# Kernel optimization log

Hardware: AMD Instinct MI355X
Metric: run time of the kernel (lower is better)

Reference implementation:

```python
import jax, jax.numpy as jnp
import numpy as np

H, D = 16, 64  # num_attention_heads, attention_head_size
BASE = 10000.0

def _rope(q, k, seq_len):
    # RotaryPositionalEmbedding: inv_freq over arange(0, D, 2); emb = cat(freqs, freqs)
    inv_freq = 1.0 / (BASE ** (jnp.arange(0, D, 2, dtype=jnp.float32) / D))  # [D/2]=32
    pos = jnp.arange(seq_len, dtype=jnp.float32)
    freqs = jnp.outer(pos, inv_freq)            # [S, 32]; equals cos_emb[..., :d]
    cos, sin = jnp.cos(freqs), jnp.sin(freqs)   # [S, 32]
    d = D // 2                                   # 32: only first half of head dim rotated
    half = d // 2                                # 16: internal rotate-half within rot part
    def rot(x):  # x: [B, H, S, D]
        xr, xp = x[..., :d], x[..., d:]
        swapped = jnp.concatenate([xr[..., half:], xr[..., :half]], axis=-1)
        xr2 = xr * cos - swapped * sin
        return jnp.concatenate([xr2, xp], axis=-1)
    return rot(q), rot(k)

def setup_inputs() -> dict:
    key = jax.random.key(0)
    ks = jax.random.split(key, 9)
    B, S, E = 2, 2048, 1024
    std = 0.02  # initializer_range
    inp = {"hidden_states": jax.random.normal(ks[0], (B, S, E), jnp.float32)}
    for i, n in enumerate(["q", "k", "v", "d"]):
        inp[f"W{n}"] = jax.random.normal(ks[1 + 2 * i], (E, E), jnp.float32) * std
        inp[f"b{n}"] = jnp.zeros((E,), jnp.float32)
    return inp

def reference(hidden_states, Wq, bq, Wk, bk, Wv, bv, Wd, bd):
    B, S, E = hidden_states.shape
    def heads(x):  # [B,S,E] -> [B,H,S,D]
        return x.reshape(B, S, H, D).transpose(0, 2, 1, 3)
    q = heads(hidden_states @ Wq + bq)
    k = heads(hidden_states @ Wk + bk)
    v = heads(hidden_states @ Wv + bv)
    q, k = _rope(q, k, S)
    scores = jnp.einsum("bhqd,bhkd->bhqk", q, k) / jnp.sqrt(jnp.float32(D))
    causal = jnp.tril(jnp.ones((S, S), dtype=bool))
    scores = jnp.where(causal, scores, -jnp.inf)
    probs = jax.nn.softmax(scores, axis=-1)
    ctx = jnp.einsum("bhqk,bhkd->bhqd", probs, v)
    ctx = ctx.transpose(0, 2, 1, 3).reshape(B, S, E)
    return ctx @ Wd + bd
```

## Files before the change

kernel.cpp:

```cpp
#include <hip/hip_runtime.h>
#include <stdint.h>

typedef __bf16 bf8 __attribute__((ext_vector_type(8)));
typedef float f4 __attribute__((ext_vector_type(4)));
typedef float f16v __attribute__((ext_vector_type(16)));
typedef unsigned short us8 __attribute__((ext_vector_type(8)));
typedef unsigned short us4 __attribute__((ext_vector_type(4)));

#define MFMA16(a, b, c) __builtin_amdgcn_mfma_f32_16x16x32_bf16(a, b, c, 0, 0, 0)
#define MFMA32(a, b, c) __builtin_amdgcn_mfma_f32_32x32x16_bf16(a, b, c, 0, 0, 0)

__device__ __forceinline__ unsigned short f2b(float f) {
  union { float f; unsigned u; } x; x.f = f;
  unsigned u = x.u;
  u += 0x7fffu + ((u >> 16) & 1u);
  return (unsigned short)(u >> 16);
}

__device__ __forceinline__ unsigned pk2(float a, float b) {
  union { float f; unsigned u; } ua, ub; ua.f = a; ub.f = b;
  return __builtin_amdgcn_perm(ub.u + 0x8000u, ua.u + 0x8000u, 0x07060302u);
}

__global__ __launch_bounds__(256) void cvt_bf16_kernel(
    const float* __restrict__ x, unsigned short* __restrict__ y) {
  int i = blockIdx.x * 256 + threadIdx.x;
  float4 v = ((const float4*)x)[i];
  us4 r = { f2b(v.x), f2b(v.y), f2b(v.z), f2b(v.w) };
  *(us4*)(y + (size_t)i * 4) = r;
}

__global__ __launch_bounds__(256) void transpose_cvt4_kernel(
    const float* __restrict__ W0, const float* __restrict__ W1,
    const float* __restrict__ W2, const float* __restrict__ W3,
    unsigned short* __restrict__ T0, unsigned short* __restrict__ T1,
    unsigned short* __restrict__ T2, unsigned short* __restrict__ T3) {
  const float* W; unsigned short* Wt;
  if (blockIdx.z == 0)      { W = W0; Wt = T0; }
  else if (blockIdx.z == 1) { W = W1; Wt = T1; }
  else if (blockIdx.z == 2) { W = W2; Wt = T2; }
  else                      { W = W3; Wt = T3; }
  __shared__ float tile[32][33];
  int tx = threadIdx.x & 31, ty = threadIdx.x >> 5;
  int kb = blockIdx.x * 32, nb = blockIdx.y * 32;
#pragma unroll
  for (int j = 0; j < 32; j += 8)
    tile[ty + j][tx] = W[(size_t)(kb + ty + j) * 1024 + nb + tx];
  __syncthreads();
#pragma unroll
  for (int j = 0; j < 32; j += 8)
    Wt[(size_t)(nb + ty + j) * 1024 + kb + tx] = f2b(tile[tx][ty + j]);
}

#define LDSK 40

__global__ __launch_bounds__(256) void gemm_qkv_kernel(
    const unsigned short* __restrict__ X,
    const unsigned short* __restrict__ Wqt, const unsigned short* __restrict__ Wkt,
    const unsigned short* __restrict__ Wvt,
    const float* __restrict__ bq, const float* __restrict__ bk,
    const float* __restrict__ bv,
    unsigned short* __restrict__ Qo, unsigned short* __restrict__ Ko,
    unsigned short* __restrict__ Vo) {
  const unsigned short* Wt; const float* bias; unsigned short* out;
  if (blockIdx.z == 0)      { Wt = Wqt; bias = bq; out = Qo; }
  else if (blockIdx.z == 1) { Wt = Wkt; bias = bk; out = Ko; }
  else                      { Wt = Wvt; bias = bv; out = Vo; }

  __shared__ unsigned short As[128 * LDSK];
  __shared__ unsigned short Bs[128 * LDSK];
  const int t = threadIdx.x;
  const int wave = t >> 6, lane = t & 63, quad = lane >> 4, l16 = lane & 15;
  const int wm = (wave >> 1) * 64, wn = (wave & 1) * 64;
  const int m0 = blockIdx.y * 128, n0 = blockIdx.x * 128;

  f4 acc[4][4];
#pragma unroll
  for (int mi = 0; mi < 4; ++mi)
#pragma unroll
    for (int ni = 0; ni < 4; ++ni) acc[mi][ni] = (f4)0.0f;

  for (int k0 = 0; k0 < 1024; k0 += 32) {
    __syncthreads();
#pragma unroll
    for (int it = 0; it < 2; ++it) {
      int chunk = t + it * 256;
      int row = chunk >> 2, c8 = (chunk & 3) * 8;
      *(us8*)&As[row * LDSK + c8] =
          *(const us8*)&X[(size_t)(m0 + row) * 1024 + k0 + c8];
      *(us8*)&Bs[row * LDSK + c8] =
          *(const us8*)&Wt[(size_t)(n0 + row) * 1024 + k0 + c8];
    }
    __syncthreads();
    bf8 a[4], b[4];
#pragma unroll
    for (int mi = 0; mi < 4; ++mi)
      a[mi] = *(const bf8*)&As[(wm + mi * 16 + l16) * LDSK + quad * 8];
#pragma unroll
    for (int ni = 0; ni < 4; ++ni)
      b[ni] = *(const bf8*)&Bs[(wn + ni * 16 + l16) * LDSK + quad * 8];
#pragma unroll
    for (int mi = 0; mi < 4; ++mi)
#pragma unroll
      for (int ni = 0; ni < 4; ++ni)
        acc[mi][ni] = MFMA16(a[mi], b[ni], acc[mi][ni]);
  }

  float biasv[4];
#pragma unroll
  for (int ni = 0; ni < 4; ++ni) biasv[ni] = bias[n0 + wn + ni * 16 + l16];

  if (blockIdx.z < 2) {
    const float kr = 13.287712379549449f / 32.0f;
    const float f0 = exp2f(-(float)l16 * kr);
    const float f1 = exp2f(-(float)(l16 + 16) * kr);
    const float qs = (blockIdx.z == 0) ? 0.18033688011112042f : 1.0f;
#pragma unroll
    for (int mi = 0; mi < 4; ++mi) {
#pragma unroll
      for (int r = 0; r < 4; ++r) {
        int m = m0 + wm + mi * 16 + quad * 4 + r;
        float s = (float)(m & 2047);
        float s0, c0, s1, c1;
        __sincosf(s * f0, &s0, &c0);
        __sincosf(s * f1, &s1, &c1);
        float v0 = acc[mi][0][r] + biasv[0];
        float v1 = acc[mi][1][r] + biasv[1];
        acc[mi][0][r] = (v0 * c0 - v1 * s0) * qs;
        acc[mi][1][r] = (v1 * c1 - v0 * s1) * qs;
        acc[mi][2][r] = (acc[mi][2][r] + biasv[2]) * qs;
        acc[mi][3][r] = (acc[mi][3][r] + biasv[3]) * qs;
      }
    }
#pragma unroll
    for (int ni = 0; ni < 4; ++ni) {
      int n = n0 + wn + ni * 16 + l16;
      int h = n >> 6, d = n & 63;
#pragma unroll
      for (int mi = 0; mi < 4; ++mi) {
#pragma unroll
        for (int r = 0; r < 4; ++r) {
          int m = m0 + wm + mi * 16 + quad * 4 + r;
          int b_ = m >> 11, s = m & 2047;
          out[(size_t)(((b_ << 4) | h) * 2048 + s) * 64 + d] = f2b(acc[mi][ni][r]);
        }
      }
    }
  } else {
#pragma unroll
    for (int ni = 0; ni < 4; ++ni) {
      int n = n0 + wn + ni * 16 + l16;
      int h = n >> 6, d = n & 63;
#pragma unroll
      for (int mi = 0; mi < 4; ++mi) {
        int m = m0 + wm + mi * 16 + quad * 4;
        int b_ = m >> 11, s = m & 2047;
        us4 w = { f2b(acc[mi][ni][0] + biasv[ni]), f2b(acc[mi][ni][1] + biasv[ni]),
                  f2b(acc[mi][ni][2] + biasv[ni]), f2b(acc[mi][ni][3] + biasv[ni]) };
        *(us4*)&out[((size_t)(((b_ << 4) | h) * 64 + d)) * 2048 + s] = w;
      }
    }
  }
}

#define PST 72

__global__ __launch_bounds__(256, 2) void flash_attn_kernel(
    const unsigned short* __restrict__ Q, const unsigned short* __restrict__ K,
    const unsigned short* __restrict__ Vt, unsigned short* __restrict__ ctx) {
  __shared__ unsigned short PsT[4][32 * PST];

  const int t = threadIdx.x;
  const int wave = t >> 6, lane = t & 63;
  const int l32 = lane & 31, hl = lane >> 5;

  const int id = blockIdx.x;
  const int bh = id & 31;
  const int j = id >> 5;
  const int qt = (j >> 3) ? (15 - (j & 7)) : (j & 7);
  const int qbase = qt * 128;
  const int b = bh >> 4, h = bh & 15;

  const unsigned short* Qh = Q + (size_t)bh * 2048 * 64;
  const unsigned short* Kh = K + (size_t)bh * 2048 * 64;
  const unsigned short* Vh = Vt + (size_t)bh * 64 * 2048;

  const int wrow0 = qbase + wave * 32;
  const int q = wrow0 + l32;

  bf8 qb[4];
#pragma unroll
  for (int c = 0; c < 4; ++c)
    qb[c] = *(const bf8*)&Qh[(size_t)q * 64 + c * 16 + hl * 8];

  f16v o0 = (f16v)0.0f, o1 = (f16v)0.0f;
  float mrow = -3e38f, lrow = 0.0f;

  unsigned short* myP = &PsT[wave][0];
  const int nkw = (wrow0 >> 6) + 1;

  bf8 kfA[2][4], vfA[2][4], kfB[2][4], vfB[2][4];

  auto loadK = [&](bf8 (&kf)[2][4], int k0) {
#pragma unroll
    for (int mt = 0; mt < 2; ++mt)
#pragma unroll
      for (int c = 0; c < 4; ++c)
        kf[mt][c] = *(const bf8*)&Kh[(size_t)(k0 + mt * 32 + l32) * 64 + c * 16 + hl * 8];
  };
  auto loadV = [&](bf8 (&vf)[2][4], int k0) {
#pragma unroll
    for (int dt = 0; dt < 2; ++dt)
#pragma unroll
      for (int c = 0; c < 4; ++c)
        vf[dt][c] = *(const bf8*)&Vh[(size_t)(dt * 32 + l32) * 2048 + k0 + c * 16 + hl * 8];
  };

  auto step = [&](int k0, bf8 (&kf)[2][4], bf8 (&vf)[2][4]) {
    f16v s0 = (f16v)0.0f, s1 = (f16v)0.0f;
#pragma unroll
    for (int c = 0; c < 4; ++c) {
      s0 = MFMA32(kf[0][c], qb[c], s0);
      s1 = MFMA32(kf[1][c], qb[c], s1);
    }
    if (k0 + 64 > wrow0) {
#pragma unroll
      for (int g = 0; g < 4; ++g)
#pragma unroll
        for (int i = 0; i < 4; ++i) {
          int kk = k0 + g * 8 + hl * 4 + i;
          if (kk > q) s0[g * 4 + i] = -3e38f;
          if (kk + 32 > q) s1[g * 4 + i] = -3e38f;
        }
    }
    float mx = fmaxf(s0[0], s1[0]);
#pragma unroll
    for (int i = 1; i < 16; ++i) mx = fmaxf(mx, fmaxf(s0[i], s1[i]));
    mx = fmaxf(mx, __shfl_xor(mx, 32));
    float mn = fmaxf(mrow, mx);
    float al = exp2f(mrow - mn);
    mrow = mn;
    float sum = 0.0f;
#pragma unroll
    for (int g = 0; g < 4; ++g) {
      float p0 = exp2f(s0[g * 4 + 0] - mn), p1 = exp2f(s0[g * 4 + 1] - mn);
      float p2 = exp2f(s0[g * 4 + 2] - mn), p3 = exp2f(s0[g * 4 + 3] - mn);
      sum += (p0 + p1) + (p2 + p3);
      uint2 w = { pk2(p0, p1), pk2(p2, p3) };
      *(uint2*)&myP[l32 * PST + g * 8 + hl * 4] = w;
      float r0 = exp2f(s1[g * 4 + 0] - mn), r1 = exp2f(s1[g * 4 + 1] - mn);
      float r2 = exp2f(s1[g * 4 + 2] - mn), r3 = exp2f(s1[g * 4 + 3] - mn);
      sum += (r0 + r1) + (r2 + r3);
      uint2 w2 = { pk2(r0, r1), pk2(r2, r3) };
      *(uint2*)&myP[l32 * PST + 32 + g * 8 + hl * 4] = w2;
    }
#pragma unroll
    for (int i = 0; i < 16; ++i) { o0[i] *= al; o1[i] *= al; }
    asm volatile("s_waitcnt lgkmcnt(0)" ::: "memory");
    bf8 pb[4];
#pragma unroll
    for (int c = 0; c < 4; ++c)
      pb[c] = *(const bf8*)&myP[l32 * PST + c * 16 + hl * 8];
#pragma unroll
    for (int c = 0; c < 4; ++c) {
      o0 = MFMA32(vf[0][c], pb[c], o0);
      o1 = MFMA32(vf[1][c], pb[c], o1);
    }
    sum += __shfl_xor(sum, 32);
    lrow = lrow * al + sum;
  };

  loadK(kfA, 0); loadV(vfA, 0);
  int kt = 0;
  while (true) {
    if (kt + 1 < nkw) { loadK(kfB, (kt + 1) * 64); loadV(vfB, (kt + 1) * 64); }
    step(kt * 64, kfA, vfA);
    ++kt; if (kt >= nkw) break;
    if (kt + 1 < nkw) { loadK(kfA, (kt + 1) * 64); loadV(vfA, (kt + 1) * 64); }
    step(kt * 64, kfB, vfB);
    ++kt; if (kt >= nkw) break;
  }

  float inv = 1.0f / lrow;
#pragma unroll
  for (int g = 0; g < 4; ++g) {
    int d0 = g * 8 + hl * 4;
    us4 w0 = { f2b(o0[g * 4 + 0] * inv), f2b(o0[g * 4 + 1] * inv),
               f2b(o0[g * 4 + 2] * inv), f2b(o0[g * 4 + 3] * inv) };
    *(us4*)&ctx[((size_t)(b * 2048 + q)) * 1024 + h * 64 + d0] = w0;
    us4 w1 = { f2b(o1[g * 4 + 0] * inv), f2b(o1[g * 4 + 1] * inv),
               f2b(o1[g * 4 + 2] * inv), f2b(o1[g * 4 + 3] * inv) };
    *(us4*)&ctx[((size_t)(b * 2048 + q)) * 1024 + h * 64 + 32 + d0] = w1;
  }
}

__global__ __launch_bounds__(256) void gemm_out_kernel(
    const unsigned short* __restrict__ A,
    const unsigned short* __restrict__ Wt,
    const float* __restrict__ bias, float* __restrict__ out) {
  __shared__ unsigned short As[128 * LDSK];
  __shared__ unsigned short Bs[128 * LDSK];
  const int t = threadIdx.x;
  const int wave = t >> 6, lane = t & 63, quad = lane >> 4, l16 = lane & 15;
  const int wm = (wave >> 1) * 64, wn = (wave & 1) * 64;
  const int m0 = blockIdx.y * 128, n0 = blockIdx.x * 128;

  f4 acc[4][4];
#pragma unroll
  for (int mi = 0; mi < 4; ++mi)
#pragma unroll
    for (int ni = 0; ni < 4; ++ni) acc[mi][ni] = (f4)0.0f;

  for (int k0 = 0; k0 < 1024; k0 += 32) {
    __syncthreads();
#pragma unroll
    for (int it = 0; it < 2; ++it) {
      int chunk = t + it * 256;
      int row = chunk >> 2, c8 = (chunk & 3) * 8;
      *(us8*)&As[row * LDSK + c8] =
          *(const us8*)&A[(size_t)(m0 + row) * 1024 + k0 + c8];
      *(us8*)&Bs[row * LDSK + c8] =
          *(const us8*)&Wt[(size_t)(n0 + row) * 1024 + k0 + c8];
    }
    __syncthreads();
    bf8 a[4], b[4];
#pragma unroll
    for (int mi = 0; mi < 4; ++mi)
      a[mi] = *(const bf8*)&As[(wm + mi * 16 + l16) * LDSK + quad * 8];
#pragma unroll
    for (int ni = 0; ni < 4; ++ni)
      b[ni] = *(const bf8*)&Bs[(wn + ni * 16 + l16) * LDSK + quad * 8];
#pragma unroll
    for (int mi = 0; mi < 4; ++mi)
#pragma unroll
      for (int ni = 0; ni < 4; ++ni)
        acc[mi][ni] = MFMA16(a[mi], b[ni], acc[mi][ni]);
  }
#pragma unroll
  for (int ni = 0; ni < 4; ++ni) {
    int n = n0 + wn + ni * 16 + l16;
    float bv_ = bias[n];
#pragma unroll
    for (int mi = 0; mi < 4; ++mi) {
#pragma unroll
      for (int r = 0; r < 4; ++r) {
        int m = m0 + wm + mi * 16 + quad * 4 + r;
        out[(size_t)m * 1024 + n] = acc[mi][ni][r] + bv_;
      }
    }
  }
}

extern "C" void kernel_launch(void* const* d_in, const int* in_sizes, int n_in,
                              void* d_out, int out_size, void* d_ws, size_t ws_size,
                              hipStream_t stream) {
  const float* hidden = (const float*)d_in[0];
  const float* Wq = (const float*)d_in[1];
  const float* bq = (const float*)d_in[2];
  const float* Wk = (const float*)d_in[3];
  const float* bk = (const float*)d_in[4];
  const float* Wv = (const float*)d_in[5];
  const float* bv = (const float*)d_in[6];
  const float* Wd = (const float*)d_in[7];
  const float* bd = (const float*)d_in[8];
  float* out = (float*)d_out;

  char* ws = (char*)d_ws;
  unsigned short* Xb  = (unsigned short*)(ws);
  unsigned short* Wqt = (unsigned short*)(ws + ( 8ull << 20));
  unsigned short* Wkt = (unsigned short*)(ws + (10ull << 20));
  unsigned short* Wvt = (unsigned short*)(ws + (12ull << 20));
  unsigned short* Wdt = (unsigned short*)(ws + (14ull << 20));
  unsigned short* Qb  = (unsigned short*)(ws + (16ull << 20));
  unsigned short* Kb  = (unsigned short*)(ws + (24ull << 20));
  unsigned short* Vb  = (unsigned short*)(ws + (32ull << 20));
  unsigned short* Cb  = (unsigned short*)(ws + (40ull << 20));

  cvt_bf16_kernel<<<4096, 256, 0, stream>>>(hidden, Xb);
  transpose_cvt4_kernel<<<dim3(32, 32, 4), 256, 0, stream>>>(
      Wq, Wk, Wv, Wd, Wqt, Wkt, Wvt, Wdt);
  gemm_qkv_kernel<<<dim3(8, 32, 3), 256, 0, stream>>>(
      Xb, Wqt, Wkt, Wvt, bq, bk, bv, Qb, Kb, Vb);
  flash_attn_kernel<<<512, 256, 0, stream>>>(Qb, Kb, Vb, Cb);
  gemm_out_kernel<<<dim3(8, 32), 256, 0, stream>>>(Cb, Wdt, bd, out);
}
```

Measured before the change: 236.1 us.

## Use direct global-to-LDS loads in GEMMs, shuffle P in registers, smaller out tiles

Both GEMM kernels now stage tiles through global_load_lds (direct global-to-LDS DMA) instead of going through registers, and drop LDS padding. The flash attention kernel removes its LDS round trip for the probability matrix by rebuilding the MFMA B operand with cross-half-wave shuffles. It also loads V just in time rather than double-buffering it, which reduces register pressure. The output GEMM switches to 64x128 tiles to launch twice as many blocks. The unpadded LDS layout risks bank conflicts, and V loads are no longer hidden behind a full step.

```diff
diff --git a/kernel.cpp b/kernel.cpp
--- a/kernel.cpp
+++ b/kernel.cpp
@@ -20,6 +20,12 @@
 __device__ __forceinline__ unsigned pk2(float a, float b) {
   union { float f; unsigned u; } ua, ub; ua.f = a; ub.f = b;
   return __builtin_amdgcn_perm(ub.u + 0x8000u, ua.u + 0x8000u, 0x07060302u);
+}
+
+__device__ __forceinline__ void gload16(const void* g, void* l) {
+  __builtin_amdgcn_global_load_lds(
+      (const __attribute__((address_space(1))) void*)g,
+      (__attribute__((address_space(3))) void*)l, 16, 0, 0);
 }
 
 __global__ __launch_bounds__(256) void cvt_bf16_kernel(
@@ -52,8 +58,6 @@
     Wt[(size_t)(nb + ty + j) * 1024 + kb + tx] = f2b(tile[tx][ty + j]);
 }
 
-#define LDSK 40
-
 __global__ __launch_bounds__(256) void gemm_qkv_kernel(
     const unsigned short* __restrict__ X,
     const unsigned short* __restrict__ Wqt, const unsigned short* __restrict__ Wkt,
@@ -67,8 +71,8 @@
   else if (blockIdx.z == 1) { Wt = Wkt; bias = bk; out = Ko; }
   else                      { Wt = Wvt; bias = bv; out = Vo; }
 
-  __shared__ unsigned short As[128 * LDSK];
-  __shared__ unsigned short Bs[128 * LDSK];
+  __shared__ unsigned short As[128 * 32];
+  __shared__ unsigned short Bs[128 * 32];
   const int t = threadIdx.x;
   const int wave = t >> 6, lane = t & 63, quad = lane >> 4, l16 = lane & 15;
   const int wm = (wave >> 1) * 64, wn = (wave & 1) * 64;
@@ -84,21 +88,21 @@
     __syncthreads();
 #pragma unroll
     for (int it = 0; it < 2; ++it) {
-      int chunk = t + it * 256;
-      int row = chunk >> 2, c8 = (chunk & 3) * 8;
-      *(us8*)&As[row * LDSK + c8] =
-          *(const us8*)&X[(size_t)(m0 + row) * 1024 + k0 + c8];
-      *(us8*)&Bs[row * LDSK + c8] =
-          *(const us8*)&Wt[(size_t)(n0 + row) * 1024 + k0 + c8];
+      int chunk = it * 256 + wave * 64 + lane;
+      int row = chunk >> 2, c = chunk & 3;
+      gload16(&X[(size_t)(m0 + row) * 1024 + k0 + c * 8],
+              &As[(size_t)(it * 256 + wave * 64) * 8]);
+      gload16(&Wt[(size_t)(n0 + row) * 1024 + k0 + c * 8],
+              &Bs[(size_t)(it * 256 + wave * 64) * 8]);
     }
     __syncthreads();
     bf8 a[4], b[4];
 #pragma unroll
     for (int mi = 0; mi < 4; ++mi)
-      a[mi] = *(const bf8*)&As[(wm + mi * 16 + l16) * LDSK + quad * 8];
+      a[mi] = *(const bf8*)&As[(wm + mi * 16 + l16) * 32 + quad * 8];
 #pragma unroll
     for (int ni = 0; ni < 4; ++ni)
-      b[ni] = *(const bf8*)&Bs[(wn + ni * 16 + l16) * LDSK + quad * 8];
+      b[ni] = *(const bf8*)&Bs[(wn + ni * 16 + l16) * 32 + quad * 8];
 #pragma unroll
     for (int mi = 0; mi < 4; ++mi)
 #pragma unroll
@@ -163,16 +167,12 @@
   }
 }
 
-#define PST 72
-
 __global__ __launch_bounds__(256, 2) void flash_attn_kernel(
     const unsigned short* __restrict__ Q, const unsigned short* __restrict__ K,
     const unsigned short* __restrict__ Vt, unsigned short* __restrict__ ctx) {
-  __shared__ unsigned short PsT[4][32 * PST];
-
   const int t = threadIdx.x;
-  const int wave = t >> 6, lane = t & 63;
-  const int l32 = lane & 31, hl = lane >> 5;
+  const int lane = t & 63;
+  const int wave = t >> 6, l32 = lane & 31, hl = lane >> 5;
 
   const int id = blockIdx.x;
   const int bh = id & 31;
@@ -195,11 +195,9 @@
 
   f16v o0 = (f16v)0.0f, o1 = (f16v)0.0f;
   float mrow = -3e38f, lrow = 0.0f;
-
-  unsigned short* myP = &PsT[wave][0];
   const int nkw = (wrow0 >> 6) + 1;
 
-  bf8 kfA[2][4], vfA[2][4], kfB[2][4], vfB[2][4];
+  bf8 kfA[2][4], kfB[2][4], vf[2][4];
 
   auto loadK = [&](bf8 (&kf)[2][4], int k0) {
 #pragma unroll
@@ -208,7 +206,7 @@
       for (int c = 0; c < 4; ++c)
         kf[mt][c] = *(const bf8*)&Kh[(size_t)(k0 + mt * 32 + l32) * 64 + c * 16 + hl * 8];
   };
-  auto loadV = [&](bf8 (&vf)[2][4], int k0) {
+  auto loadV = [&](int k0) {
 #pragma unroll
     for (int dt = 0; dt < 2; ++dt)
 #pragma unroll
@@ -216,7 +214,7 @@
         vf[dt][c] = *(const bf8*)&Vh[(size_t)(dt * 32 + l32) * 2048 + k0 + c * 16 + hl * 8];
   };
 
-  auto step = [&](int k0, bf8 (&kf)[2][4], bf8 (&vf)[2][4]) {
+  auto step = [&](int k0, bf8 (&kf)[2][4]) {
     f16v s0 = (f16v)0.0f, s1 = (f16v)0.0f;
 #pragma unroll
     for (int c = 0; c < 4; ++c) {
@@ -240,44 +238,48 @@
     float mn = fmaxf(mrow, mx);
     float al = exp2f(mrow - mn);
     mrow = mn;
+    uint2 pd2[8];
     float sum = 0.0f;
 #pragma unroll
     for (int g = 0; g < 4; ++g) {
       float p0 = exp2f(s0[g * 4 + 0] - mn), p1 = exp2f(s0[g * 4 + 1] - mn);
       float p2 = exp2f(s0[g * 4 + 2] - mn), p3 = exp2f(s0[g * 4 + 3] - mn);
       sum += (p0 + p1) + (p2 + p3);
-      uint2 w = { pk2(p0, p1), pk2(p2, p3) };
-      *(uint2*)&myP[l32 * PST + g * 8 + hl * 4] = w;
+      pd2[g].x = pk2(p0, p1); pd2[g].y = pk2(p2, p3);
       float r0 = exp2f(s1[g * 4 + 0] - mn), r1 = exp2f(s1[g * 4 + 1] - mn);
       float r2 = exp2f(s1[g * 4 + 2] - mn), r3 = exp2f(s1[g * 4 + 3] - mn);
       sum += (r0 + r1) + (r2 + r3);
-      uint2 w2 = { pk2(r0, r1), pk2(r2, r3) };
-      *(uint2*)&myP[l32 * PST + 32 + g * 8 + hl * 4] = w2;
+      pd2[4 + g].x = pk2(r0, r1); pd2[4 + g].y = pk2(r2, r3);
     }
 #pragma unroll
     for (int i = 0; i < 16; ++i) { o0[i] *= al; o1[i] *= al; }
-    asm volatile("s_waitcnt lgkmcnt(0)" ::: "memory");
-    bf8 pb[4];
-#pragma unroll
-    for (int c = 0; c < 4; ++c)
-      pb[c] = *(const bf8*)&myP[l32 * PST + c * 16 + hl * 8];
 #pragma unroll
     for (int c = 0; c < 4; ++c) {
-      o0 = MFMA32(vf[0][c], pb[c], o0);
-      o1 = MFMA32(vf[1][c], pb[c], o1);
+      uint2 lo = pd2[2 * c], hi = pd2[2 * c + 1];
+      unsigned sx = hl ? lo.x : hi.x, sy = hl ? lo.y : hi.y;
+      unsigned rx = __shfl_xor(sx, 32), ry = __shfl_xor(sy, 32);
+      union { uint4 u; bf8 v; } fr;
+      fr.u.x = hl ? rx : lo.x;
+      fr.u.y = hl ? ry : lo.y;
+      fr.u.z = hl ? hi.x : rx;
+      fr.u.w = hl ? hi.y : ry;
+      o0 = MFMA32(vf[0][c], fr.v, o0);
+      o1 = MFMA32(vf[1][c], fr.v, o1);
     }
     sum += __shfl_xor(sum, 32);
     lrow = lrow * al + sum;
   };
 
-  loadK(kfA, 0); loadV(vfA, 0);
+  loadK(kfA, 0);
   int kt = 0;
   while (true) {
-    if (kt + 1 < nkw) { loadK(kfB, (kt + 1) * 64); loadV(vfB, (kt + 1) * 64); }
-    step(kt * 64, kfA, vfA);
+    loadV(kt * 64);
+    if (kt + 1 < nkw) loadK(kfB, (kt + 1) * 64);
+    step(kt * 64, kfA);
     ++kt; if (kt >= nkw) break;
-    if (kt + 1 < nkw) { loadK(kfA, (kt + 1) * 64); loadV(vfA, (kt + 1) * 64); }
-    step(kt * 64, kfB, vfB);
+    loadV(kt * 64);
+    if (kt + 1 < nkw) loadK(kfA, (kt + 1) * 64);
+    step(kt * 64, kfB);
     ++kt; if (kt >= nkw) break;
   }
 
@@ -298,40 +300,44 @@
     const unsigned short* __restrict__ A,
     const unsigned short* __restrict__ Wt,
     const float* __restrict__ bias, float* __restrict__ out) {
-  __shared__ unsigned short As[128 * LDSK];
-  __shared__ unsigned short Bs[128 * LDSK];
+  __shared__ unsigned short As[64 * 32];
+  __shared__ unsigned short Bs[128 * 32];
   const int t = threadIdx.x;
   const int wave = t >> 6, lane = t & 63, quad = lane >> 4, l16 = lane & 15;
-  const int wm = (wave >> 1) * 64, wn = (wave & 1) * 64;
-  const int m0 = blockIdx.y * 128, n0 = blockIdx.x * 128;
-
-  f4 acc[4][4];
-#pragma unroll
-  for (int mi = 0; mi < 4; ++mi)
+  const int wm = (wave & 1) * 32, wn = (wave >> 1) * 64;
+  const int m0 = blockIdx.y * 64, n0 = blockIdx.x * 128;
+
+  f4 acc[2][4];
+#pragma unroll
+  for (int mi = 0; mi < 2; ++mi)
 #pragma unroll
     for (int ni = 0; ni < 4; ++ni) acc[mi][ni] = (f4)0.0f;
 
   for (int k0 = 0; k0 < 1024; k0 += 32) {
     __syncthreads();
-#pragma unroll
-    for (int it = 0; it < 2; ++it) {
-      int chunk = t + it * 256;
-      int row = chunk >> 2, c8 = (chunk & 3) * 8;
-      *(us8*)&As[row * LDSK + c8] =
-          *(const us8*)&A[(size_t)(m0 + row) * 1024 + k0 + c8];
-      *(us8*)&Bs[row * LDSK + c8] =
-          *(const us8*)&Wt[(size_t)(n0 + row) * 1024 + k0 + c8];
+    {
+      int chunk = wave * 64 + lane;
+      int row = chunk >> 2, c = chunk & 3;
+      gload16(&A[(size_t)(m0 + row) * 1024 + k0 + c * 8],
+              &As[(size_t)(wave * 64) * 8]);
+#pragma unroll
+      for (int it = 0; it < 2; ++it) {
+        int ch = it * 256 + wave * 64 + lane;
+        int rw = ch >> 2, cc = ch & 3;
+        gload16(&Wt[(size_t)(n0 + rw) * 1024 + k0 + cc * 8],
+                &Bs[(size_t)(it * 256 + wave * 64) * 8]);
+      }
     }
     __syncthreads();
-    bf8 a[4], b[4];
-#pragma unroll
-    for (int mi = 0; mi < 4; ++mi)
-      a[mi] = *(const bf8*)&As[(wm + mi * 16 + l16) * LDSK + quad * 8];
+    bf8 a[2], b[4];
+#pragma unroll
+    for (int mi = 0; mi < 2; ++mi)
+      a[mi] = *(const bf8*)&As[(wm + mi * 16 + l16) * 32 + quad * 8];
 #pragma unroll
     for (int ni = 0; ni < 4; ++ni)
-      b[ni] = *(const bf8*)&Bs[(wn + ni * 16 + l16) * LDSK + quad * 8];
-#pragma unroll
-    for (int mi = 0; mi < 4; ++mi)
+      b[ni] = *(const bf8*)&Bs[(wn + ni * 16 + l16) * 32 + quad * 8];
+#pragma unroll
+    for (int mi = 0; mi < 2; ++mi)
 #pragma unroll
       for (int ni = 0; ni < 4; ++ni)
         acc[mi][ni] = MFMA16(a[mi], b[ni], acc[mi][ni]);
@@ -341,7 +347,7 @@
     int n = n0 + wn + ni * 16 + l16;
     float bv_ = bias[n];
 #pragma unroll
-    for (int mi = 0; mi < 4; ++mi) {
+    for (int mi = 0; mi < 2; ++mi) {
 #pragma unroll
       for (int r = 0; r < 4; ++r) {
         int m = m0 + wm + mi * 16 + quad * 4 + r;
@@ -382,5 +388,5 @@
   gemm_qkv_kernel<<<dim3(8, 32, 3), 256, 0, stream>>>(
       Xb, Wqt, Wkt, Wvt, bq, bk, bv, Qb, Kb, Vb);
   flash_attn_kernel<<<512, 256, 0, stream>>>(Qb, Kb, Vb, Cb);
-  gemm_out_kernel<<<dim3(8, 32), 256, 0, stream>>>(Cb, Wdt, bd, out);
-}
+  gemm_out_kernel<<<dim3(8, 64), 256, 0, stream>>>(Cb, Wdt, bd, out);
+}
```

Result: faster. 225.3 us (-4.5%).
